# Performance work log

Hardware: AMD Instinct MI355X
Metric: run time of the kernel (lower is better)

## Reference

```python
import jax, jax.numpy as jnp
import numpy as np

B, F, M, D = 64, 4, 4096, 1024
ITERS = 15

def _sign(x):
    # bipolar quantize: sign with sign(0) = +1
    return jnp.where(x >= 0, 1.0, -1.0).astype(x.dtype)

def setup_inputs() -> dict:
    key = jax.random.key(0)
    k1, k2, k3 = jax.random.split(key, 3)
    # bipolar (+1/-1) hypervectors, MAP/software VSA
    input = _sign(jax.random.normal(k1, (B, D), dtype=jnp.float32))
    init_estimates = _sign(jax.random.normal(k2, (B, F, D), dtype=jnp.float32))
    codebooks = _sign(jax.random.normal(k3, (F, M, D), dtype=jnp.float32))
    return {"input": input, "init_estimates": init_estimates, "codebooks": codebooks}

def reference(input, init_estimates, codebooks):
    # Concurrent resonator network (bipolar MAP VSA):
    #  bind = elementwise multiply, inverse = identity, multibind = product over factors.
    #  inv_others[b,f,:] = prod_{j != f} estimates[b,j,:] == (prod_all) * estimates  (since e*e = 1)
    def step(carry, _):
        est, converged, iters = carry
        total = jnp.prod(est, axis=-2, keepdims=True)          # (b,1,d)
        inv_others = total * est                                # (b,f,d) product of the other factors
        new_est = input[:, None, :] * inv_others                # unbind: (b,f,d)
        sim = jnp.einsum('bfd,fmd->bfm', new_est, codebooks)    # dot similarity vs each codebook
        upd = _sign(jnp.einsum('bfm,fmd->bfd', sim, codebooks)) # multiset weighted bundle + quantize
        now_conv = jnp.all(upd == est)                          # estimates stopped changing
        est2 = jnp.where(converged, est, upd)                   # freeze after convergence
        iters2 = iters + jnp.where(converged, 0, 1)
        return (est2, converged | now_conv, iters2), None

    init = (init_estimates, jnp.array(False), jnp.array(0, jnp.int32))
    (est, conv, iters), _ = jax.lax.scan(step, init, None, length=ITERS)
    # cleanup: argmax(|similarity|) per factor -> codebook indices
    sim = jnp.einsum('bfd,fmd->bfm', est, codebooks)
    outcome = jnp.argmax(jnp.abs(sim), axis=-1)                 # (b,f) int
    return outcome, est, iters, conv
```

## Files before the change

kernel.cpp:

```cpp
#include <hip/hip_runtime.h>
#include <hip/hip_fp16.h>

#define B_ 64
#define F_ 4
#define M_ 4096
#define D_ 1024
#define W_ 16
#define CW_ 64
#define NITER 15
#define NBLK 64
#define FPAD 32

typedef _Float16 f16;
typedef _Float16 f16x8 __attribute__((ext_vector_type(8)));
typedef float f32x4 __attribute__((ext_vector_type(4)));
typedef unsigned int u32;
typedef unsigned short u16;
typedef unsigned long long u64;

#define LD_AG(p)     __hip_atomic_load((p), __ATOMIC_RELAXED, __HIP_MEMORY_SCOPE_AGENT)
#define ST_AG(p, v)  __hip_atomic_store((p), (v), __ATOMIC_RELAXED, __HIP_MEMORY_SCOPE_AGENT)

__device__ __align__(16) u64 g_cbBits[F_ * M_ * W_];
__device__ __align__(16) u64 g_colBits[F_ * D_ * CW_];
__device__ __align__(16) f16 g_G[F_ * D_ * D_];
__device__ __align__(16) u64 g_inBits[B_ * W_];
__device__ __align__(16) u64 g_est[2][W_ * F_ * B_];
__device__ int g_done[NITER][NBLK * FPAD];
__device__ int g_mism[NITER][NBLK * FPAD];

__device__ __forceinline__ u32 nib16(u32 x) {
    x &= 0x0F0F0F0Fu;
    x = (x | (x >> 4)) & 0x00FF00FFu;
    x = (x | (x >> 8)) & 0x0000FFFFu;
    return x;
}

__global__ __launch_bounds__(256) void k_pack(const float* __restrict__ inp,
                                              const float* __restrict__ est0,
                                              const float* __restrict__ cb) {
    __shared__ unsigned char nib[4096];
    int blk = blockIdx.x, tid = threadIdx.x;
    int wv = tid >> 6, lane = tid & 63;
    const float* src; u64* dst; int r0; int estmode = 0;
    if (blk < 1024)      { src = cb;   dst = g_cbBits; r0 = blk * 16; }
    else if (blk < 1040) { src = est0; dst = g_est[0]; r0 = (blk - 1024) * 16; estmode = 1; }
    else if (blk < 1044) { src = inp;  dst = g_inBits; r0 = (blk - 1040) * 16; }
    else {
        int idx = (blk - 1044) * 256 + tid;
        const int n = NITER * NBLK * FPAD;
        if (idx < n) ((int*)g_done)[idx] = 0;
        else if (idx < 2 * n) ((int*)g_mism)[idx - n] = 0;
        return;
    }
    int rw = r0 + wv * 4;
    unsigned char* mynib = nib + wv * 1024;
    #pragma unroll
    for (int rr = 0; rr < 4; rr++) {
        const float4* s4 = (const float4*)(src + (size_t)(rw + rr) * D_);
        #pragma unroll
        for (int it = 0; it < 4; it++) {
            float4 v = s4[it * 64 + lane];
            u32 n = (__float_as_uint(v.x) >> 31)
                  | (((__float_as_uint(v.y) >> 31)) << 1)
                  | (((__float_as_uint(v.z) >> 31)) << 2)
                  | (((__float_as_uint(v.w) >> 31)) << 3);
            mynib[rr * 256 + it * 64 + lane] = (unsigned char)n;
        }
    }
    uint4 q = *(const uint4*)(mynib + (lane >> 4) * 256 + (lane & 15) * 16);
    u32 w0 = nib16(q.x), w1 = nib16(q.y), w2 = nib16(q.z), w3 = nib16(q.w);
    u64 word = (u64)(w0 | (w1 << 16)) | ((u64)(w2 | (w3 << 16)) << 32);
    int r = rw + (lane >> 4), w = lane & 15;
    size_t oi = estmode ? (size_t)((w * 4 + (r & 3)) * 64 + (r >> 2))
                        : (size_t)r * W_ + w;
    dst[oi] = word;
}

__global__ __launch_bounds__(256) void k_bitT() {
    int tid = threadIdx.x, wv = tid >> 6, lane = tid & 63;
    int tbase = (blockIdx.x * 4 + wv) * 4;
    for (int q = 0; q < 4; q++) {
        int task = tbase + q;
        int mt = task & 63;
        int wd = (task >> 6) & 15;
        int f  = task >> 10;
        u64 row = g_cbBits[((size_t)(f * M_ + mt * 64 + lane)) * W_ + wd];
        u64 myout = 0;
        #pragma unroll
        for (int j = 0; j < 64; j++) {
            u64 t = __ballot((row >> j) & 1ULL);
            if (lane == j) myout = t;
        }
        g_colBits[((size_t)(f * D_ + wd * 64 + lane)) * CW_ + mt] = myout;
    }
}

__global__ __launch_bounds__(256) void k_G() {
    int blk = blockIdx.x;
    int f = blk / 136;
    int pi = blk % 136;
    int t1 = 0;
    while (pi >= 16 - t1) { pi -= 16 - t1; t1++; }
    int t2 = t1 + pi;
    __shared__ u64 L1T[64][64];
    __shared__ u64 L2T[64][64];
    int tid = threadIdx.x;
    int wv = tid >> 6, lane = tid & 63;
    for (int it = 0; it < 16; it++) {
        int w = it * 4 + wv;
        L1T[w][lane] = g_colBits[((size_t)(f * D_ + t1 * 64 + lane)) * CW_ + w];
        L2T[w][lane] = g_colBits[((size_t)(f * D_ + t2 * 64 + lane)) * CW_ + w];
    }
    __syncthreads();
    int g1 = tid >> 4, g2 = tid & 15;
    int p[4][4] = {};
    for (int w = 0; w < 64; w++) {
        u64 a0 = L1T[w][g1], a1 = L1T[w][g1 + 16], a2 = L1T[w][g1 + 32], a3 = L1T[w][g1 + 48];
        u64 b0 = L2T[w][g2], b1 = L2T[w][g2 + 16], b2 = L2T[w][g2 + 32], b3 = L2T[w][g2 + 48];
        p[0][0] += __popcll(a0 ^ b0); p[0][1] += __popcll(a0 ^ b1);
        p[0][2] += __popcll(a0 ^ b2); p[0][3] += __popcll(a0 ^ b3);
        p[1][0] += __popcll(a1 ^ b0); p[1][1] += __popcll(a1 ^ b1);
        p[1][2] += __popcll(a1 ^ b2); p[1][3] += __popcll(a1 ^ b3);
        p[2][0] += __popcll(a2 ^ b0); p[2][1] += __popcll(a2 ^ b1);
        p[2][2] += __popcll(a2 ^ b2); p[2][3] += __popcll(a2 ^ b3);
        p[3][0] += __popcll(a3 ^ b0); p[3][1] += __popcll(a3 ^ b1);
        p[3][2] += __popcll(a3 ^ b2); p[3][3] += __popcll(a3 ^ b3);
    }
    #pragma unroll
    for (int i = 0; i < 4; i++) {
        int d1 = t1 * 64 + g1 + 16 * i;
        #pragma unroll
        for (int j = 0; j < 4; j++) {
            int d2 = t2 * 64 + g2 + 16 * j;
            g_G[((size_t)(f * D_ + d1)) * D_ + d2] = (f16)(M_ - 2 * p[i][j]);
        }
    }
    if (t1 == t2) return;
    __syncthreads();
    f16* Lt = (f16*)L1T;
    #pragma unroll
    for (int i = 0; i < 4; i++)
        #pragma unroll
        for (int j = 0; j < 4; j++)
            Lt[(g2 + 16 * j) * 72 + (g1 + 16 * i)] = (f16)(M_ - 2 * p[i][j]);
    __syncthreads();
    int r = tid >> 2, c0 = (tid & 3) * 16;
    const uint4* s = (const uint4*)&Lt[r * 72 + c0];
    uint4 v0 = s[0], v1 = s[1];
    uint4* dsto = (uint4*)&g_G[((size_t)(f * D_ + t2 * 64 + r)) * D_ + t1 * 64 + c0];
    dsto[0] = v0; dsto[1] = v1;
}

__device__ __forceinline__ u32 pairval(u32 bits, int i) {
    return 0x3C003C00u | (((bits >> i) & 1u) << 15) | (((bits >> (i + 1)) & 1u) << 31);
}

__global__ __launch_bounds__(256) void k_loop(float* __restrict__ out) {
    int blk = blockIdx.x;
    int f = blk & 3, dg = blk >> 2;
    int tid = threadIdx.x;
    int wv = tid >> 6, lane = tid & 63;
    __shared__ u64 neL[64][17];
    __shared__ u64 inL[64][17];
    __shared__ __align__(16) char ldsB[64 * 2048];
    __shared__ int red[256];
    {
        const char* gsrc = (const char*)(g_G + ((size_t)(f * D_ + dg * 64)) * D_);
        for (int i = tid; i < 8192; i += 256) {
            int row = i >> 7, col = i & 127;
            uint4 v = *(const uint4*)(gsrc + (size_t)row * 2048 + col * 16);
            *(uint4*)(ldsB + row * 2048 + ((col * 16) ^ ((row & 7) << 4))) = v;
        }
        for (int i = tid; i < 1024; i += 256)
            inL[i >> 4][i & 15] = g_inBits[i];
    }
    const unsigned char* neB = (const unsigned char*)neL;
    int dd = lane & 15, gg = lane >> 4;
    int aBase = (wv * 16 + dd) * 136 + gg;
    int nb = tid & 63, wq = tid >> 6;
    u64 prev[4];
    if (dd == 0) {
        #pragma unroll
        for (int j = 0; j < 4; j++)
            prev[j] = g_est[0][(dg * 4 + f) * 64 + (wv * 16 + gg * 4 + j)];
    }
    for (int t = 0; t < NITER; t++) {
        const u64* rb = g_est[t & 1];
        u64* wb = g_est[(t + 1) & 1];
        {
            const char* base0 = (const char*)rb + (size_t)wq * 8192 + (size_t)nb * 8;
            const char* base1 = base0 + 4096;
            u64 e00, e01, e02, e03, e10, e11, e12, e13;
            u64 e20, e21, e22, e23, e30, e31, e32, e33;
            asm volatile(
                "global_load_dwordx2 %0, %16, off sc0 sc1\n\t"
                "global_load_dwordx2 %1, %16, off offset:512 sc0 sc1\n\t"
                "global_load_dwordx2 %2, %16, off offset:1024 sc0 sc1\n\t"
                "global_load_dwordx2 %3, %16, off offset:1536 sc0 sc1\n\t"
                "global_load_dwordx2 %4, %16, off offset:2048 sc0 sc1\n\t"
                "global_load_dwordx2 %5, %16, off offset:2560 sc0 sc1\n\t"
                "global_load_dwordx2 %6, %16, off offset:3072 sc0 sc1\n\t"
                "global_load_dwordx2 %7, %16, off offset:3584 sc0 sc1\n\t"
                "global_load_dwordx2 %8, %17, off sc0 sc1\n\t"
                "global_load_dwordx2 %9, %17, off offset:512 sc0 sc1\n\t"
                "global_load_dwordx2 %10, %17, off offset:1024 sc0 sc1\n\t"
                "global_load_dwordx2 %11, %17, off offset:1536 sc0 sc1\n\t"
                "global_load_dwordx2 %12, %17, off offset:2048 sc0 sc1\n\t"
                "global_load_dwordx2 %13, %17, off offset:2560 sc0 sc1\n\t"
                "global_load_dwordx2 %14, %17, off offset:3072 sc0 sc1\n\t"
                "global_load_dwordx2 %15, %17, off offset:3584 sc0 sc1\n\t"
                "s_waitcnt vmcnt(0)"
                : "=&v"(e00), "=&v"(e01), "=&v"(e02), "=&v"(e03),
                  "=&v"(e10), "=&v"(e11), "=&v"(e12), "=&v"(e13),
                  "=&v"(e20), "=&v"(e21), "=&v"(e22), "=&v"(e23),
                  "=&v"(e30), "=&v"(e31), "=&v"(e32), "=&v"(e33)
                : "v"(base0), "v"(base1)
                : "memory");
            u64 x0 = inL[nb][wq * 4 + 0] ^ e00 ^ e01 ^ e02 ^ e03;
            u64 x1 = inL[nb][wq * 4 + 1] ^ e10 ^ e11 ^ e12 ^ e13;
            u64 x2 = inL[nb][wq * 4 + 2] ^ e20 ^ e21 ^ e22 ^ e23;
            u64 x3 = inL[nb][wq * 4 + 3] ^ e30 ^ e31 ^ e32 ^ e33;
            u64 f0 = (f == 0) ? e00 : (f == 1) ? e01 : (f == 2) ? e02 : e03;
            u64 f1 = (f == 0) ? e10 : (f == 1) ? e11 : (f == 2) ? e12 : e13;
            u64 f2 = (f == 0) ? e20 : (f == 1) ? e21 : (f == 2) ? e22 : e23;
            u64 f3 = (f == 0) ? e30 : (f == 1) ? e31 : (f == 2) ? e32 : e33;
            neL[nb][wq * 4 + 0] = x0 ^ f0;
            neL[nb][wq * 4 + 1] = x1 ^ f1;
            neL[nb][wq * 4 + 2] = x2 ^ f2;
            neL[nb][wq * 4 + 3] = x3 ^ f3;
        }
        __syncthreads();
        f32x4 acc[4][2] = {};
        #pragma unroll
        for (int c = 0; c < 32; c++) {
            u32 bits = neB[aBase + c * 4];
            f16x8 a;
            ((u32*)&a)[0] = pairval(bits, 0);
            ((u32*)&a)[1] = pairval(bits, 2);
            ((u32*)&a)[2] = pairval(bits, 4);
            ((u32*)&a)[3] = pairval(bits, 6);
            #pragma unroll
            for (int ct = 0; ct < 4; ct++) {
                int rowB = ct * 16 + dd;
                f16x8 bf = *(const f16x8*)(ldsB + rowB * 2048 +
                                           ((c * 64 + gg * 16) ^ ((rowB & 7) << 4)));
                acc[ct][c & 1] =
                    __builtin_amdgcn_mfma_f32_16x16x32_f16(a, bf, acc[ct][c & 1], 0, 0, 0);
            }
        }
        u64 msk[4][4];
        #pragma unroll
        for (int ct = 0; ct < 4; ct++)
            #pragma unroll
            for (int j = 0; j < 4; j++) {
                float v = acc[ct][0][j] + acc[ct][1][j];
                msk[ct][j] = __ballot(v < 0.0f);
            }
        int mm = 0;
        if (dd == 0) {
            #pragma unroll
            for (int j = 0; j < 4; j++) {
                int b = wv * 16 + gg * 4 + j;
                u64 nv = ((msk[0][j] >> (gg * 16)) & 0xFFFFu)
                       | (((msk[1][j] >> (gg * 16)) & 0xFFFFu) << 16)
                       | (((msk[2][j] >> (gg * 16)) & 0xFFFFu) << 32)
                       | (((msk[3][j] >> (gg * 16)) & 0xFFFFu) << 48);
                if (prev[j] != nv) mm = 1;
                prev[j] = nv;
                ST_AG(&wb[(dg * 4 + f) * 64 + b], nv);
            }
        }
        u64 anym = __ballot(mm != 0);
        if (lane == 0 && anym)
            ST_AG(&g_mism[t][blk * FPAD + wv], 1);
        __syncthreads();
        if (tid == 0)
            ST_AG(&g_done[t][blk * FPAD], 1);
        if (tid < NBLK) {
            while (LD_AG(&g_done[t][tid * FPAD]) == 0) {}
        }
        __syncthreads();
    }
    const u64* eb_g = g_est[NITER & 1];
    if (blk == 0 && tid < NBLK) {
        int anyt[NITER];
        #pragma unroll
        for (int t = 0; t < NITER; t++) {
            const int* mp = &g_mism[t][tid * FPAD];
            int v = LD_AG(&mp[0]) | LD_AG(&mp[1]) | LD_AG(&mp[2]) | LD_AG(&mp[3]);
            anyt[t] = (__ballot(v != 0) != 0);
        }
        if (tid == 0) {
            int iters = 0, conv = 0;
            #pragma unroll
            for (int t = 0; t < NITER; t++) {
                if (!conv) iters++;
                if (!anyt[t]) conv = 1;
            }
            out[256 + 262144] = (float)iters;
            out[256 + 262144 + 1] = (float)conv;
        }
    }
    for (int s = 0; s < 4; s++) {
        int task = blk * 4 + s;
        int bb = task >> 2, ff = task & 3;
        for (int j = 0; j < 4; j++) {
            int d = j * 256 + tid;
            u64 w = LD_AG(&eb_g[((d >> 6) * 4 + ff) * 64 + bb]);
            out[256 + ((size_t)(bb * 4 + ff)) * D_ + d] = ((w >> (d & 63)) & 1) ? -1.0f : 1.0f;
        }
        u64 eb[W_];
        #pragma unroll
        for (int w = 0; w < W_; w++) eb[w] = LD_AG(&eb_g[(w * 4 + ff) * 64 + bb]);
        int bestKey = -1;
        for (int j = 0; j < 16; j++) {
            int m = j * 256 + tid;
            int p = 0;
            #pragma unroll
            for (int w = 0; w < W_; w++)
                p += __popcll(eb[w] ^ g_cbBits[((size_t)(ff * M_ + m)) * W_ + w]);
            int sv = D_ - 2 * p;
            int a = sv < 0 ? -sv : sv;
            int key = (a << 12) | (4095 - m);
            if (key > bestKey) bestKey = key;
        }
        red[tid] = bestKey;
        __syncthreads();
        for (int off = 128; off > 0; off >>= 1) {
            if (tid < off) red[tid] = max(red[tid], red[tid + off]);
            __syncthreads();
        }
        if (tid == 0) out[bb * 4 + ff] = (float)(4095 - (red[0] & 0xFFF));
        __syncthreads();
    }
}

extern "C" void kernel_launch(void* const* d_in, const int* in_sizes, int n_in,
                              void* d_out, int out_size, void* d_ws, size_t ws_size,
                              hipStream_t stream) {
    (void)d_ws; (void)ws_size;
    const float* inp  = (const float*)d_in[0];
    const float* est0 = (const float*)d_in[1];
    const float* cb   = (const float*)d_in[2];
    float* out = (float*)d_out;

    int flagInts = 2 * NITER * NBLK * FPAD;
    int zeroBlks = (flagInts + 255) / 256;
    k_pack<<<1044 + zeroBlks, 256, 0, stream>>>(inp, est0, cb);
    k_bitT<<<256, 256, 0, stream>>>();
    k_G<<<544, 256, 0, stream>>>();
    k_loop<<<NBLK, 256, 0, stream>>>(out);
}
```

Measured before the change: 303.4 us.

## Replace global barrier with per-producer flags and slot-per-iteration estimate exchange

Swaps the all-block barrier at the end of each resonator iteration for per-producer ready flags. Each iteration's estimates go into their own slot, so a consumer waits only for the 48 producers it needs and can move ahead without waiting for everyone. Estimate gathering now uses wide dwordx4 loads plus LDS atomicXor accumulation. The k_G popcount kernel also stages its shared tiles in two halves to use less LDS. This adds LDS atomic traffic and more slot memory, and correctness depends on the flag protocol.

```diff
diff --git a/kernel.cpp b/kernel.cpp
--- a/kernel.cpp
+++ b/kernel.cpp
@@ -8,8 +8,9 @@
 #define W_ 16
 #define CW_ 64
 #define NITER 15
+#define NSLOT 16
 #define NBLK 64
-#define FPAD 32
+#define FPAD 16
 
 typedef _Float16 f16;
 typedef _Float16 f16x8 __attribute__((ext_vector_type(8)));
@@ -25,8 +26,8 @@
 __device__ __align__(16) u64 g_colBits[F_ * D_ * CW_];
 __device__ __align__(16) f16 g_G[F_ * D_ * D_];
 __device__ __align__(16) u64 g_inBits[B_ * W_];
-__device__ __align__(16) u64 g_est[2][W_ * F_ * B_];
-__device__ int g_done[NITER][NBLK * FPAD];
+__device__ __align__(16) u64 g_ex[NSLOT][64][64];
+__device__ int g_fl[NSLOT][64 * FPAD];
 __device__ int g_mism[NITER][NBLK * FPAD];
 
 __device__ __forceinline__ u32 nib16(u32 x) {
@@ -42,15 +43,16 @@
     __shared__ unsigned char nib[4096];
     int blk = blockIdx.x, tid = threadIdx.x;
     int wv = tid >> 6, lane = tid & 63;
-    const float* src; u64* dst; int r0; int estmode = 0;
-    if (blk < 1024)      { src = cb;   dst = g_cbBits; r0 = blk * 16; }
-    else if (blk < 1040) { src = est0; dst = g_est[0]; r0 = (blk - 1024) * 16; estmode = 1; }
-    else if (blk < 1044) { src = inp;  dst = g_inBits; r0 = (blk - 1040) * 16; }
+    const float* src; int r0; int mode;
+    if (blk < 1024)      { src = cb;   r0 = blk * 16;          mode = 0; }
+    else if (blk < 1040) { src = est0; r0 = (blk - 1024) * 16; mode = 1; }
+    else if (blk < 1044) { src = inp;  r0 = (blk - 1040) * 16; mode = 2; }
     else {
         int idx = (blk - 1044) * 256 + tid;
-        const int n = NITER * NBLK * FPAD;
-        if (idx < n) ((int*)g_done)[idx] = 0;
-        else if (idx < 2 * n) ((int*)g_mism)[idx - n] = 0;
+        const int n1 = NSLOT * 64 * FPAD;
+        const int n2 = NITER * NBLK * FPAD;
+        if (idx < n1) ((int*)g_fl)[idx] = 0;
+        else if (idx < n1 + n2) ((int*)g_mism)[idx - n1] = 0;
         return;
     }
     int rw = r0 + wv * 4;
@@ -72,9 +74,12 @@
     u32 w0 = nib16(q.x), w1 = nib16(q.y), w2 = nib16(q.z), w3 = nib16(q.w);
     u64 word = (u64)(w0 | (w1 << 16)) | ((u64)(w2 | (w3 << 16)) << 32);
     int r = rw + (lane >> 4), w = lane & 15;
-    size_t oi = estmode ? (size_t)((w * 4 + (r & 3)) * 64 + (r >> 2))
-                        : (size_t)r * W_ + w;
-    dst[oi] = word;
+    if (mode == 0)      g_cbBits[(size_t)r * W_ + w] = word;
+    else if (mode == 2) g_inBits[r * W_ + w] = word;
+    else {
+        int b = r >> 2, ff = r & 3;
+        g_ex[0][ff * 16 + w][b] = word;
+    }
 }
 
 __global__ __launch_bounds__(256) void k_bitT() {
@@ -103,29 +108,32 @@
     int t1 = 0;
     while (pi >= 16 - t1) { pi -= 16 - t1; t1++; }
     int t2 = t1 + pi;
-    __shared__ u64 L1T[64][64];
-    __shared__ u64 L2T[64][64];
+    __shared__ u64 L1T[32][64];
+    __shared__ u64 L2T[32][64];
     int tid = threadIdx.x;
     int wv = tid >> 6, lane = tid & 63;
-    for (int it = 0; it < 16; it++) {
-        int w = it * 4 + wv;
-        L1T[w][lane] = g_colBits[((size_t)(f * D_ + t1 * 64 + lane)) * CW_ + w];
-        L2T[w][lane] = g_colBits[((size_t)(f * D_ + t2 * 64 + lane)) * CW_ + w];
-    }
-    __syncthreads();
     int g1 = tid >> 4, g2 = tid & 15;
     int p[4][4] = {};
-    for (int w = 0; w < 64; w++) {
-        u64 a0 = L1T[w][g1], a1 = L1T[w][g1 + 16], a2 = L1T[w][g1 + 32], a3 = L1T[w][g1 + 48];
-        u64 b0 = L2T[w][g2], b1 = L2T[w][g2 + 16], b2 = L2T[w][g2 + 32], b3 = L2T[w][g2 + 48];
-        p[0][0] += __popcll(a0 ^ b0); p[0][1] += __popcll(a0 ^ b1);
-        p[0][2] += __popcll(a0 ^ b2); p[0][3] += __popcll(a0 ^ b3);
-        p[1][0] += __popcll(a1 ^ b0); p[1][1] += __popcll(a1 ^ b1);
-        p[1][2] += __popcll(a1 ^ b2); p[1][3] += __popcll(a1 ^ b3);
-        p[2][0] += __popcll(a2 ^ b0); p[2][1] += __popcll(a2 ^ b1);
-        p[2][2] += __popcll(a2 ^ b2); p[2][3] += __popcll(a2 ^ b3);
-        p[3][0] += __popcll(a3 ^ b0); p[3][1] += __popcll(a3 ^ b1);
-        p[3][2] += __popcll(a3 ^ b2); p[3][3] += __popcll(a3 ^ b3);
+    for (int wh = 0; wh < 2; wh++) {
+        for (int it = 0; it < 8; it++) {
+            int w = it * 4 + wv;
+            L1T[w][lane] = g_colBits[((size_t)(f * D_ + t1 * 64 + lane)) * CW_ + wh * 32 + w];
+            L2T[w][lane] = g_colBits[((size_t)(f * D_ + t2 * 64 + lane)) * CW_ + wh * 32 + w];
+        }
+        __syncthreads();
+        for (int w = 0; w < 32; w++) {
+            u64 a0 = L1T[w][g1], a1 = L1T[w][g1 + 16], a2 = L1T[w][g1 + 32], a3 = L1T[w][g1 + 48];
+            u64 b0 = L2T[w][g2], b1 = L2T[w][g2 + 16], b2 = L2T[w][g2 + 32], b3 = L2T[w][g2 + 48];
+            p[0][0] += __popcll(a0 ^ b0); p[0][1] += __popcll(a0 ^ b1);
+            p[0][2] += __popcll(a0 ^ b2); p[0][3] += __popcll(a0 ^ b3);
+            p[1][0] += __popcll(a1 ^ b0); p[1][1] += __popcll(a1 ^ b1);
+            p[1][2] += __popcll(a1 ^ b2); p[1][3] += __popcll(a1 ^ b3);
+            p[2][0] += __popcll(a2 ^ b0); p[2][1] += __popcll(a2 ^ b1);
+            p[2][2] += __popcll(a2 ^ b2); p[2][3] += __popcll(a2 ^ b3);
+            p[3][0] += __popcll(a3 ^ b0); p[3][1] += __popcll(a3 ^ b1);
+            p[3][2] += __popcll(a3 ^ b2); p[3][3] += __popcll(a3 ^ b3);
+        }
+        __syncthreads();
     }
     #pragma unroll
     for (int i = 0; i < 4; i++) {
@@ -162,7 +170,7 @@
     int tid = threadIdx.x;
     int wv = tid >> 6, lane = tid & 63;
     __shared__ u64 neL[64][17];
-    __shared__ u64 inL[64][17];
+    __shared__ u64 inL[64][16];
     __shared__ __align__(16) char ldsB[64 * 2048];
     __shared__ int red[256];
     {
@@ -176,59 +184,62 @@
             inL[i >> 4][i & 15] = g_inBits[i];
     }
     const unsigned char* neB = (const unsigned char*)neL;
+    unsigned long long* nf = (unsigned long long*)neL;
     int dd = lane & 15, gg = lane >> 4;
     int aBase = (wv * 16 + dd) * 136 + gg;
-    int nb = tid & 63, wq = tid >> 6;
+    int myp = f * 16 + dg;
+    int q = tid >> 2, sub = tid & 3;
+    int fp = q >> 4; if (fp >= f) fp++;
+    int gp = fp * 16 + (q & 15);
     u64 prev[4];
     if (dd == 0) {
         #pragma unroll
         for (int j = 0; j < 4; j++)
-            prev[j] = g_est[0][(dg * 4 + f) * 64 + (wv * 16 + gg * 4 + j)];
-    }
+            prev[j] = LD_AG(&g_ex[0][myp][wv * 16 + gg * 4 + j]);
+    }
+    __syncthreads();
     for (int t = 0; t < NITER; t++) {
-        const u64* rb = g_est[t & 1];
-        u64* wb = g_est[(t + 1) & 1];
         {
-            const char* base0 = (const char*)rb + (size_t)wq * 8192 + (size_t)nb * 8;
-            const char* base1 = base0 + 4096;
-            u64 e00, e01, e02, e03, e10, e11, e12, e13;
-            u64 e20, e21, e22, e23, e30, e31, e32, e33;
+            int c0 = tid * 4;
+            #pragma unroll
+            for (int k = 0; k < 4; k++) {
+                int c = c0 + k;
+                neL[c >> 4][c & 15] = inL[c >> 4][c & 15];
+            }
+        }
+        __syncthreads();
+        if (tid < 192) {
+            if (t) { while (LD_AG(&g_fl[t][gp * FPAD]) == 0) {} }
+            const char* bb = (const char*)&g_ex[t][gp][sub * 16];
+            uint4 r0, r1, r2, r3, r4, r5, r6, r7;
             asm volatile(
-                "global_load_dwordx2 %0, %16, off sc0 sc1\n\t"
-                "global_load_dwordx2 %1, %16, off offset:512 sc0 sc1\n\t"
-                "global_load_dwordx2 %2, %16, off offset:1024 sc0 sc1\n\t"
-                "global_load_dwordx2 %3, %16, off offset:1536 sc0 sc1\n\t"
-                "global_load_dwordx2 %4, %16, off offset:2048 sc0 sc1\n\t"
-                "global_load_dwordx2 %5, %16, off offset:2560 sc0 sc1\n\t"
-                "global_load_dwordx2 %6, %16, off offset:3072 sc0 sc1\n\t"
-                "global_load_dwordx2 %7, %16, off offset:3584 sc0 sc1\n\t"
-                "global_load_dwordx2 %8, %17, off sc0 sc1\n\t"
-                "global_load_dwordx2 %9, %17, off offset:512 sc0 sc1\n\t"
-                "global_load_dwordx2 %10, %17, off offset:1024 sc0 sc1\n\t"
-                "global_load_dwordx2 %11, %17, off offset:1536 sc0 sc1\n\t"
-                "global_load_dwordx2 %12, %17, off offset:2048 sc0 sc1\n\t"
-                "global_load_dwordx2 %13, %17, off offset:2560 sc0 sc1\n\t"
-                "global_load_dwordx2 %14, %17, off offset:3072 sc0 sc1\n\t"
-                "global_load_dwordx2 %15, %17, off offset:3584 sc0 sc1\n\t"
+                "global_load_dwordx4 %0, %8, off sc0 sc1\n\t"
+                "global_load_dwordx4 %1, %8, off offset:16 sc0 sc1\n\t"
+                "global_load_dwordx4 %2, %8, off offset:32 sc0 sc1\n\t"
+                "global_load_dwordx4 %3, %8, off offset:48 sc0 sc1\n\t"
+                "global_load_dwordx4 %4, %8, off offset:64 sc0 sc1\n\t"
+                "global_load_dwordx4 %5, %8, off offset:80 sc0 sc1\n\t"
+                "global_load_dwordx4 %6, %8, off offset:96 sc0 sc1\n\t"
+                "global_load_dwordx4 %7, %8, off offset:112 sc0 sc1\n\t"
                 "s_waitcnt vmcnt(0)"
-                : "=&v"(e00), "=&v"(e01), "=&v"(e02), "=&v"(e03),
-                  "=&v"(e10), "=&v"(e11), "=&v"(e12), "=&v"(e13),
-                  "=&v"(e20), "=&v"(e21), "=&v"(e22), "=&v"(e23),
-                  "=&v"(e30), "=&v"(e31), "=&v"(e32), "=&v"(e33)
-                : "v"(base0), "v"(base1)
+                : "=&v"(r0), "=&v"(r1), "=&v"(r2), "=&v"(r3),
+                  "=&v"(r4), "=&v"(r5), "=&v"(r6), "=&v"(r7)
+                : "v"(bb)
                 : "memory");
-            u64 x0 = inL[nb][wq * 4 + 0] ^ e00 ^ e01 ^ e02 ^ e03;
-            u64 x1 = inL[nb][wq * 4 + 1] ^ e10 ^ e11 ^ e12 ^ e13;
-            u64 x2 = inL[nb][wq * 4 + 2] ^ e20 ^ e21 ^ e22 ^ e23;
-            u64 x3 = inL[nb][wq * 4 + 3] ^ e30 ^ e31 ^ e32 ^ e33;
-            u64 f0 = (f == 0) ? e00 : (f == 1) ? e01 : (f == 2) ? e02 : e03;
-            u64 f1 = (f == 0) ? e10 : (f == 1) ? e11 : (f == 2) ? e12 : e13;
-            u64 f2 = (f == 0) ? e20 : (f == 1) ? e21 : (f == 2) ? e22 : e23;
-            u64 f3 = (f == 0) ? e30 : (f == 1) ? e31 : (f == 2) ? e32 : e33;
-            neL[nb][wq * 4 + 0] = x0 ^ f0;
-            neL[nb][wq * 4 + 1] = x1 ^ f1;
-            neL[nb][wq * 4 + 2] = x2 ^ f2;
-            neL[nb][wq * 4 + 3] = x3 ^ f3;
+            int wp = gp & 15;
+            int bb0 = sub * 16;
+            u64 d[16];
+            d[0]=r0.x|((u64)r0.y<<32); d[1]=r0.z|((u64)r0.w<<32);
+            d[2]=r1.x|((u64)r1.y<<32); d[3]=r1.z|((u64)r1.w<<32);
+            d[4]=r2.x|((u64)r2.y<<32); d[5]=r2.z|((u64)r2.w<<32);
+            d[6]=r3.x|((u64)r3.y<<32); d[7]=r3.z|((u64)r3.w<<32);
+            d[8]=r4.x|((u64)r4.y<<32); d[9]=r4.z|((u64)r4.w<<32);
+            d[10]=r5.x|((u64)r5.y<<32); d[11]=r5.z|((u64)r5.w<<32);
+            d[12]=r6.x|((u64)r6.y<<32); d[13]=r6.z|((u64)r6.w<<32);
+            d[14]=r7.x|((u64)r7.y<<32); d[15]=r7.z|((u64)r7.w<<32);
+            #pragma unroll
+            for (int k = 0; k < 16; k++)
+                atomicXor(&nf[(bb0 + k) * 17 + wp], d[k]);
         }
         __syncthreads();
         f32x4 acc[4][2] = {};
@@ -268,7 +279,7 @@
                        | (((msk[3][j] >> (gg * 16)) & 0xFFFFu) << 48);
                 if (prev[j] != nv) mm = 1;
                 prev[j] = nv;
-                ST_AG(&wb[(dg * 4 + f) * 64 + b], nv);
+                ST_AG(&g_ex[t + 1][myp][b], nv);
             }
         }
         u64 anym = __ballot(mm != 0);
@@ -276,13 +287,10 @@
             ST_AG(&g_mism[t][blk * FPAD + wv], 1);
         __syncthreads();
         if (tid == 0)
-            ST_AG(&g_done[t][blk * FPAD], 1);
-        if (tid < NBLK) {
-            while (LD_AG(&g_done[t][tid * FPAD]) == 0) {}
-        }
-        __syncthreads();
-    }
-    const u64* eb_g = g_est[NITER & 1];
+            ST_AG(&g_fl[t + 1][myp * FPAD], 1);
+    }
+    if (tid < 64) { while (LD_AG(&g_fl[NITER][tid * FPAD]) == 0) {} }
+    __syncthreads();
     if (blk == 0 && tid < NBLK) {
         int anyt[NITER];
         #pragma unroll
@@ -307,12 +315,12 @@
         int bb = task >> 2, ff = task & 3;
         for (int j = 0; j < 4; j++) {
             int d = j * 256 + tid;
-            u64 w = LD_AG(&eb_g[((d >> 6) * 4 + ff) * 64 + bb]);
+            u64 w = LD_AG(&g_ex[NITER][ff * 16 + (d >> 6)][bb]);
             out[256 + ((size_t)(bb * 4 + ff)) * D_ + d] = ((w >> (d & 63)) & 1) ? -1.0f : 1.0f;
         }
         u64 eb[W_];
         #pragma unroll
-        for (int w = 0; w < W_; w++) eb[w] = LD_AG(&eb_g[(w * 4 + ff) * 64 + bb]);
+        for (int w = 0; w < W_; w++) eb[w] = LD_AG(&g_ex[NITER][ff * 16 + w][bb]);
         int bestKey = -1;
         for (int j = 0; j < 16; j++) {
             int m = j * 256 + tid;
@@ -345,7 +353,7 @@
     const float* cb   = (const float*)d_in[2];
     float* out = (float*)d_out;
 
-    int flagInts = 2 * NITER * NBLK * FPAD;
+    int flagInts = NSLOT * 64 * FPAD + NITER * NBLK * FPAD;
     int zeroBlks = (flagInts + 255) / 256;
     k_pack<<<1044 + zeroBlks, 256, 0, stream>>>(inp, est0, cb);
     k_bitT<<<256, 256, 0, stream>>>();
```

Result: faster. 296.1 us (-2.4%).
